# Kernel tuning notes

Hardware: AMD Instinct MI355X
Metric: run time of the kernel (lower is better)

Reference implementation:

```python
import jax, jax.numpy as jnp
import numpy as np

B, T, HID, H, Dk, Dv, K = 2, 1024, 1024, 8, 128, 128, 4
EPS = 1e-5


def _dwconv_causal(y, w, b):
    # y: [B,T,C], w: [C,1,K], b: [C]; torch Conv1d(padding=K-1) then [:, :, :T] == causal left-pad
    C = y.shape[-1]
    z = jnp.transpose(y, (0, 2, 1))  # [B,C,T]
    z = jax.lax.conv_general_dilated(
        z, w, window_strides=(1,), padding=[(K - 1, 0)],
        feature_group_count=C, dimension_numbers=("NCH", "OIH", "NCH"))
    z = z + b[None, :, None]
    return jnp.transpose(z, (0, 2, 1))


def _forward(x, Wq, Wk, Wv, conv_q_w, conv_q_b, conv_k_w, conv_k_b,
             conv_v_w, conv_v_b, Wa, ba, Wb, bb, Wg, Wo, ln_g, ln_b):
    b_, t_ = x.shape[0], x.shape[1]
    q = jax.nn.silu(_dwconv_causal(x @ Wq, conv_q_w, conv_q_b))
    k = jax.nn.silu(_dwconv_causal(x @ Wk, conv_k_w, conv_k_b))
    v = jax.nn.silu(_dwconv_causal(x @ Wv, conv_v_w, conv_v_b))
    q = q.reshape(b_, t_, H, Dk)
    k = k.reshape(b_, t_, H, Dk) * (Dk ** -0.5)
    v = v.reshape(b_, t_, H, Dv)
    alpha = jax.nn.sigmoid(x @ Wa + ba)  # [B,T,H]
    beta = jax.nn.sigmoid(x @ Wb + bb)   # [B,T,H]

    # time-major for scan
    qt = jnp.transpose(q, (1, 0, 2, 3))  # [T,B,H,Dk]
    kt = jnp.transpose(k, (1, 0, 2, 3))
    vt = jnp.transpose(v, (1, 0, 2, 3))  # [T,B,H,Dv]
    at = jnp.transpose(alpha, (1, 0, 2))  # [T,B,H]
    bt = jnp.transpose(beta, (1, 0, 2))

    def step(S, inp):
        q_t, k_t, v_t, a_t, b_t = inp
        sk = jnp.einsum('bhij,bhj->bhi', S, k_t)          # S @ k
        err = sk - v_t                                     # [B,H,Dv]
        S = a_t[:, :, None, None] * S - b_t[:, :, None, None] * (err[..., None] * k_t[:, :, None, :])
        o_t = jnp.einsum('bhij,bhj->bhi', S, q_t)          # S @ q (post-update)
        return S, o_t

    S0 = jnp.zeros((b_, H, Dv, Dk), x.dtype)
    _, o = jax.lax.scan(step, S0, (qt, kt, vt, at, bt))
    o = jnp.transpose(o, (1, 0, 2, 3))  # [B,T,H,Dv]

    # LayerNorm over Dv
    mu = jnp.mean(o, axis=-1, keepdims=True)
    var = jnp.mean((o - mu) ** 2, axis=-1, keepdims=True)
    o = (o - mu) * jax.lax.rsqrt(var + EPS) * ln_g + ln_b

    g = jax.nn.sigmoid(x @ Wg).reshape(b_, t_, H, Dv)
    o = (o * g).reshape(b_, t_, H * Dv)
    return o @ Wo


def setup_inputs() -> dict:
    key = jax.random.key(0)
    ks = jax.random.split(key, 18)
    s = 0.02

    def n(k, shape, scale=s):
        return jax.random.normal(k, shape, jnp.float32) * scale

    return {
        "x": jax.random.normal(ks[0], (B, T, HID), jnp.float32),
        "Wq": n(ks[1], (HID, H * Dk)),
        "Wk": n(ks[2], (HID, H * Dk)),
        "Wv": n(ks[3], (HID, H * Dv)),
        "conv_q_w": n(ks[4], (H * Dk, 1, K), 0.25),
        "conv_q_b": n(ks[5], (H * Dk,), 0.1),
        "conv_k_w": n(ks[6], (H * Dk, 1, K), 0.25),
        "conv_k_b": n(ks[7], (H * Dk,), 0.1),
        "conv_v_w": n(ks[8], (H * Dv, 1, K), 0.25),
        "conv_v_b": n(ks[9], (H * Dv,), 0.1),
        "Wa": n(ks[10], (HID, H)),
        "ba": n(ks[11], (H,), 0.1),
        "Wb": n(ks[12], (HID, H)),
        "bb": n(ks[13], (H,), 0.1),
        "Wg": n(ks[14], (HID, H * Dv)),
        "Wo": n(ks[15], (H * Dv, HID)),
        "ln_g": jnp.ones((Dv,), jnp.float32),
        "ln_b": jnp.zeros((Dv,), jnp.float32),
    }


def reference(x, Wq, Wk, Wv, conv_q_w, conv_q_b, conv_k_w, conv_k_b,
              conv_v_w, conv_v_b, Wa, ba, Wb, bb, Wg, Wo, ln_g, ln_b):
    return _forward(x, Wq, Wk, Wv, conv_q_w, conv_q_b, conv_k_w, conv_k_b,
                    conv_v_w, conv_v_b, Wa, ba, Wb, bb, Wg, Wo, ln_g, ln_b)
```

## Files before the change

### kernel.cpp

```cpp
#include <hip/hip_runtime.h>

#define TSEQ 1024
#define HID_ 1024
#define NH 8
#define DK 128
#define DV 128
#define ROWS 2048
#define SZf (ROWS * HID_)
#define LCH 64
#define NCK 16
#define KSTR 136
#define ESTR 65

typedef __attribute__((ext_vector_type(8))) short short8;
typedef __attribute__((ext_vector_type(4))) float f32x4;
#define MFMA __builtin_amdgcn_mfma_f32_16x16x32_bf16

__device__ __forceinline__ float sig_(float x) { return 1.f / (1.f + __expf(-x)); }

__device__ __forceinline__ ushort f2bf(float f) {
    unsigned int u = __builtin_bit_cast(unsigned int, f);
    u += 0x7FFF + ((u >> 16) & 1);
    return (ushort)(u >> 16);
}
__device__ __forceinline__ unsigned int pk2(float lo, float hi) {
    return (unsigned int)f2bf(lo) | ((unsigned int)f2bf(hi) << 16);
}

__global__ __launch_bounds__(256)
void k_wT(const float* __restrict__ s0, const float* __restrict__ s1,
          const float* __restrict__ s2, const float* __restrict__ s3,
          ushort* __restrict__ dst)
{
    const int z = blockIdx.z;
    const float* W = (z == 0) ? s0 : (z == 1) ? s1 : (z == 2) ? s2 : s3;
    ushort* WT = dst + (size_t)z * (1024 * 1024);
    __shared__ float t[64][65];
    const int n0 = blockIdx.x * 64, k0 = blockIdx.y * 64;
    const int rr = threadIdx.x >> 4, cc = threadIdx.x & 15;
#pragma unroll
    for (int i = 0; i < 4; ++i) {
        const int row = i * 16 + rr;
        float4 v = *(const float4*)(W + (size_t)(k0 + row) * 1024 + n0 + cc * 4);
        t[row][cc * 4 + 0] = v.x; t[row][cc * 4 + 1] = v.y;
        t[row][cc * 4 + 2] = v.z; t[row][cc * 4 + 3] = v.w;
    }
    __syncthreads();
#pragma unroll
    for (int i = 0; i < 4; ++i) {
        const int n = i * 16 + rr;
        const int kc = cc * 4;
        ushort4 o;
        o.x = f2bf(t[kc + 0][n]); o.y = f2bf(t[kc + 1][n]);
        o.z = f2bf(t[kc + 2][n]); o.w = f2bf(t[kc + 3][n]);
        *(ushort4*)(WT + (size_t)(n0 + n) * 1024 + k0 + kc) = o;
    }
}

#define LDSB 40
__device__ __forceinline__ void gemm_tile_mfma(const float* __restrict__ A,
                                               const ushort* __restrict__ BT,
                                               float* __restrict__ C,
                                               int brow, int bcol)
{
    __shared__ ushort As[128 * LDSB];
    __shared__ ushort Bs[128 * LDSB];
    const int tid  = threadIdx.x;
    const int lane = tid & 63;
    const int wv   = tid >> 6;
    const int wm   = (wv >> 1) * 64;
    const int wn   = (wv & 1) * 64;
    const int l15  = lane & 15;
    const int k8   = (lane >> 4) * 8;
    const int srow = tid >> 1;
    const int skh  = (tid & 1) * 16;

    f32x4 acc[4][4];
#pragma unroll
    for (int i = 0; i < 4; ++i)
#pragma unroll
        for (int j = 0; j < 4; ++j)
#pragma unroll
            for (int e = 0; e < 4; ++e) acc[i][j][e] = 0.f;

    const float*  arow = A  + (size_t)(brow + srow) * 1024 + skh;
    const ushort* brp  = BT + (size_t)(bcol + srow) * 1024 + skh;
    ushort* asw = As + srow * LDSB + skh;
    ushort* bsw = Bs + srow * LDSB + skh;

    for (int k0 = 0; k0 < 1024; k0 += 32) {
        float4 a0 = *(const float4*)(arow + k0);
        float4 a1 = *(const float4*)(arow + k0 + 4);
        float4 a2 = *(const float4*)(arow + k0 + 8);
        float4 a3 = *(const float4*)(arow + k0 + 12);
        uint4 b0 = *(const uint4*)(brp + k0);
        uint4 b1 = *(const uint4*)(brp + k0 + 8);
        uint4 w0, w1;
        w0.x = pk2(a0.x, a0.y); w0.y = pk2(a0.z, a0.w);
        w0.z = pk2(a1.x, a1.y); w0.w = pk2(a1.z, a1.w);
        w1.x = pk2(a2.x, a2.y); w1.y = pk2(a2.z, a2.w);
        w1.z = pk2(a3.x, a3.y); w1.w = pk2(a3.z, a3.w);
        __syncthreads();
        *(uint4*)(asw)     = w0;
        *(uint4*)(asw + 8) = w1;
        *(uint4*)(bsw)     = b0;
        *(uint4*)(bsw + 8) = b1;
        __syncthreads();
        short8 af[4], bf[4];
#pragma unroll
        for (int i = 0; i < 4; ++i)
            af[i] = *(const short8*)(As + (wm + i * 16 + l15) * LDSB + k8);
#pragma unroll
        for (int j = 0; j < 4; ++j)
            bf[j] = *(const short8*)(Bs + (wn + j * 16 + l15) * LDSB + k8);
#pragma unroll
        for (int i = 0; i < 4; ++i)
#pragma unroll
            for (int j = 0; j < 4; ++j)
                acc[i][j] = MFMA(af[i], bf[j], acc[i][j], 0, 0, 0);
    }
    const int l4 = lane >> 4;
#pragma unroll
    for (int i = 0; i < 4; ++i)
#pragma unroll
        for (int j = 0; j < 4; ++j)
#pragma unroll
            for (int r = 0; r < 4; ++r)
                C[(size_t)(brow + wm + i * 16 + l4 * 4 + r) * 1024 +
                  bcol + wn + j * 16 + l15] = acc[i][j][r];
}

__global__ __launch_bounds__(256)
void k_gemm4(const float* __restrict__ A, const ushort* __restrict__ WT,
             float* __restrict__ Cbase)
{
    const ushort* BT = WT + (size_t)blockIdx.z * (1024 * 1024);
    float* C = Cbase + (size_t)blockIdx.z * SZf;
    gemm_tile_mfma(A, BT, C, blockIdx.y * 128, blockIdx.x * 128);
}

__global__ __launch_bounds__(256)
void k_gemm1(const float* __restrict__ A, const ushort* __restrict__ BT,
             float* __restrict__ C)
{
    gemm_tile_mfma(A, BT, C, blockIdx.y * 128, blockIdx.x * 128);
}

__global__ __launch_bounds__(64)
void k_ab(const float* __restrict__ x, const float* __restrict__ Wa,
          const float* __restrict__ ba, const float* __restrict__ Wb,
          const float* __restrict__ bb, float* __restrict__ aT,
          float* __restrict__ bT)
{
    const int r = blockIdx.x;
    const int lane = threadIdx.x;
    const int b = r >> 10, t = r & 1023;
    const float* xr = x + (size_t)r * HID_;
    float acc[16];
#pragma unroll
    for (int n = 0; n < 16; ++n) acc[n] = 0.f;
    for (int c = lane; c < HID_; c += 64) {
        const float xv = xr[c];
        const float* wa = Wa + c * 8;
        const float* wb = Wb + c * 8;
#pragma unroll
        for (int n = 0; n < 8; ++n) {
            acc[n]     = fmaf(xv, wa[n], acc[n]);
            acc[8 + n] = fmaf(xv, wb[n], acc[8 + n]);
        }
    }
#pragma unroll
    for (int n = 0; n < 16; ++n) {
#pragma unroll
        for (int m = 32; m; m >>= 1) acc[n] += __shfl_xor(acc[n], m);
    }
    if (lane < 8) {
        aT[(size_t)(b * 8 + lane) * TSEQ + t] = sig_(acc[lane] + ba[lane]);
        bT[(size_t)(b * 8 + lane) * TSEQ + t] = sig_(acc[8 + lane] + bb[lane]);
    }
}

__global__ __launch_bounds__(256)
void k_conv_save(const float* __restrict__ q, const float* __restrict__ k,
                 const float* __restrict__ v, float* __restrict__ scr)
{
    const int z = blockIdx.z, b = blockIdx.y, j = blockIdx.x + 1;
    const float* y = (z == 0) ? q : (z == 1) ? k : v;
    float* d = scr + ((size_t)(z * 2 + b) * 15 + (j - 1)) * 3 * 1024;
    const float* s = y + ((size_t)b * TSEQ + j * 64 - 3) * HID_;
    for (int i = threadIdx.x; i < 3 * 1024; i += 256)
        d[i] = s[i];
}

__global__ __launch_bounds__(256)
void k_conv_apply(float* __restrict__ q, float* __restrict__ k, float* __restrict__ v,
                  const float* __restrict__ scr,
                  const float* __restrict__ wq, const float* __restrict__ bq,
                  const float* __restrict__ wk, const float* __restrict__ bk,
                  const float* __restrict__ wv, const float* __restrict__ bv)
{
    const int z = blockIdx.z, b = blockIdx.y;
    const int j = blockIdx.x >> 2, cg = blockIdx.x & 3;
    float* y          = (z == 0) ? q  : (z == 1) ? k  : v;
    const float* w    = (z == 0) ? wq : (z == 1) ? wk : wv;
    const float* bias = (z == 0) ? bq : (z == 1) ? bk : bv;
    const float scale = (z == 1) ? 0.08838834764831845f : 1.f;
    const int c = cg * 256 + threadIdx.x;
    const float w0 = w[c * 4], w1 = w[c * 4 + 1], w2 = w[c * 4 + 2], w3 = w[c * 4 + 3];
    const float bs = bias[c];
    float y0 = 0.f, y1 = 0.f, y2 = 0.f;
    if (j > 0) {
        const float* s = scr + ((size_t)(z * 2 + b) * 15 + (j - 1)) * 3 * 1024 + c;
        y0 = s[0]; y1 = s[1024]; y2 = s[2048];
    }
    float* yp = y + ((size_t)b * TSEQ + j * 64) * HID_ + c;
#pragma unroll 4
    for (int t = 0; t < 64; ++t) {
        float y3  = yp[(size_t)t * HID_];
        float acc = fmaf(w0, y0, fmaf(w1, y1, fmaf(w2, y2, fmaf(w3, y3, bs))));
        float sv  = acc * sig_(acc) * scale;
        yp[(size_t)t * HID_] = sv;
        y0 = y1; y1 = y2; y2 = y3;
    }
}

__global__ __launch_bounds__(256)
void k_prep(const float* __restrict__ klin, const float* __restrict__ qlin,
            const float* __restrict__ aT, const float* __restrict__ bT,
            ushort* __restrict__ Mg, ushort* __restrict__ Gg,
            float* __restrict__ pug, float* __restrict__ pog,
            float* __restrict__ cg, float* __restrict__ dtotg)
{
    const int cid = blockIdx.x;
    const int bh = cid >> 4, c = cid & 15;
    const int b = bh >> 3, h = bh & 7;
    const int tid = threadIdx.x;
    const int t0 = c * LCH;

    __shared__ ushort Kb[64 * KSTR], Qb[64 * KSTR];
    __shared__ float Ef[64 * ESTR];
    __shared__ float Mf[64 * ESTR];
    __shared__ float cums[64], bv[64];

    if (tid < 64) {
        const float a = aT[(size_t)bh * TSEQ + t0 + tid];
        bv[tid] = bT[(size_t)bh * TSEQ + t0 + tid];
        float cs = __logf(a);
#pragma unroll
        for (int d = 1; d < 64; d <<= 1) {
            float pv = __shfl_up(cs, d);
            if (tid >= d) cs += pv;
        }
        cums[tid] = cs;
    }
    const float* kb = klin + ((size_t)b * TSEQ + t0) * HID_ + h * DK;
    const float* qb = qlin + ((size_t)b * TSEQ + t0) * HID_ + h * DK;
#pragma unroll
    for (int j = 0; j < 8; ++j) {
        const int i4 = tid + j * 256;
        const int row = i4 >> 5, c4 = i4 & 31;
        float4 kv = *(const float4*)(kb + (size_t)row * HID_ + c4 * 4);
        float4 qv = *(const float4*)(qb + (size_t)row * HID_ + c4 * 4);
        uint2 kp; kp.x = pk2(kv.x, kv.y); kp.y = pk2(kv.z, kv.w);
        uint2 qp; qp.x = pk2(qv.x, qv.y); qp.y = pk2(qv.z, qv.w);
        *(uint2*)(Kb + row * KSTR + c4 * 4) = kp;
        *(uint2*)(Qb + row * KSTR + c4 * 4) = qp;
    }
    __syncthreads();

    const int wv = tid >> 6, l = tid & 63, l15 = l & 15, lq = l >> 4;
    const int k8o = lq * 8;
    f32x4 accK[4], accQ4[4];
#pragma unroll
    for (int j = 0; j < 4; ++j) {
        accK[j] = f32x4{0.f, 0.f, 0.f, 0.f};
        accQ4[j] = f32x4{0.f, 0.f, 0.f, 0.f};
    }
#pragma unroll
    for (int kk = 0; kk < 4; ++kk) {
        short8 aK = *(const short8*)(Kb + (wv * 16 + l15) * KSTR + kk * 32 + k8o);
        short8 aQ = *(const short8*)(Qb + (wv * 16 + l15) * KSTR + kk * 32 + k8o);
#pragma unroll
        for (int js = 0; js < 4; ++js) {
            short8 bK = *(const short8*)(Kb + (js * 16 + l15) * KSTR + kk * 32 + k8o);
            accK[js]  = MFMA(aK, bK, accK[js], 0, 0, 0);
            accQ4[js] = MFMA(aQ, bK, accQ4[js], 0, 0, 0);
        }
    }
    ushort* Gc = Gg + (size_t)cid * 4096;
#pragma unroll
    for (int js = 0; js < 4; ++js) {
#pragma unroll
        for (int r = 0; r < 4; ++r) {
            const int t = wv * 16 + lq * 4 + r;
            const int s = js * 16 + l15;
            const float cp = (t > 0) ? cums[t - 1] : 0.f;
            Ef[t * ESTR + s] = (s < t) ? __expf(cp - cums[s]) * accK[js][r] : 0.f;
            const float gv = (s <= t) ? __expf(cums[t] - cums[s]) * accQ4[js][r] : 0.f;
            Gc[t * 64 + s] = f2bf(gv);
        }
    }
    __syncthreads();

    if (tid < 64) {
        const int s = tid;
        for (int r = 0; r < 64; ++r) Mf[r * ESTR + s] = 0.f;
        Mf[s * ESTR + s] = bv[s];
        for (int t = 1; t < 64; ++t) {
            float s0 = 0.f, s1 = 0.f;
            int r = 0;
            for (; r + 1 < t; r += 2) {
                s0 = fmaf(Ef[t * ESTR + r],     Mf[r * ESTR + s],       s0);
                s1 = fmaf(Ef[t * ESTR + r + 1], Mf[(r + 1) * ESTR + s], s1);
            }
            if (r < t) s0 = fmaf(Ef[t * ESTR + r], Mf[r * ESTR + s], s0);
            if (s < t) Mf[t * ESTR + s] = -bv[t] * (s0 + s1);
        }
    }
    __syncthreads();
    ushort* Mc = Mg + (size_t)cid * 4096;
#pragma unroll
    for (int j = 0; j < 16; ++j) {
        const int e = tid + j * 256;
        Mc[e] = f2bf(Mf[(e >> 6) * ESTR + (e & 63)]);
    }
    if (tid < 64) {
        const float cp = (tid > 0) ? cums[tid - 1] : 0.f;
        pug[cid * 64 + tid] = __expf(cp);
        pog[cid * 64 + tid] = __expf(cums[tid]);
        cg [cid * 64 + tid] = __expf(cums[63] - cums[tid]);
        if (tid == 0) dtotg[cid] = __expf(cums[63]);
    }
}

__global__ __launch_bounds__(256)
void k_scan2(const float* __restrict__ klin, const float* __restrict__ qlin,
             const float* __restrict__ vlin,
             const ushort* __restrict__ Mg, const ushort* __restrict__ Gg,
             const float* __restrict__ pug, const float* __restrict__ pog,
             const float* __restrict__ cg, const float* __restrict__ dtotg,
             float* __restrict__ o)
{
    const int blk = blockIdx.x;
    const int bh = blk >> 2, rb = blk & 3;
    const int b = bh >> 3, h = bh & 7;
    const int tid = threadIdx.x;
    const int wv = tid >> 6, l = tid & 63, l15 = l & 15, lq = l >> 4;
    const int k8o = lq * 8;

    __shared__ ushort Kb[64 * KSTR], Qb[64 * KSTR];
    __shared__ ushort KTb[128 * 72];
    __shared__ float  Vtf[32 * 72];
    __shared__ ushort Mb[64 * 72], Gb[64 * 72];
    __shared__ ushort Shb[32 * KSTR], Slb[32 * KSTR];
    __shared__ ushort Yb[32 * 72], Wb[32 * 72], Wcb[32 * 72];
    __shared__ float  Otf[64 * 36];
    __shared__ float  puv[64], pov[64], cv2[64], dts[1];

    const int trow  = wv >> 1;
    const int tcol0 = (wv & 1) * 2;
    const int scol0 = (wv & 1) * 4;

    f32x4 accS[4];
#pragma unroll
    for (int m = 0; m < 4; ++m) accS[m] = f32x4{0.f, 0.f, 0.f, 0.f};

    const float* kbase = klin + (size_t)b * TSEQ * HID_ + h * DK;
    const float* qbase = qlin + (size_t)b * TSEQ * HID_ + h * DK;
    const float* vbase = vlin + (size_t)b * TSEQ * HID_ + h * DV + rb * 32;
    float* obase = o + (size_t)bh * TSEQ * DV + rb * 32;

    for (int c = 0; c < NCK; ++c) {
        const int cid = bh * 16 + c;
        const int t0 = c * LCH;
#pragma unroll
        for (int j = 0; j < 8; ++j) {
            const int i4 = tid + j * 256;
            const int row = i4 >> 5, c4 = i4 & 31;
            float4 kv = *(const float4*)(kbase + (size_t)(t0 + row) * HID_ + c4 * 4);
            float4 qv = *(const float4*)(qbase + (size_t)(t0 + row) * HID_ + c4 * 4);
            uint2 kp; kp.x = pk2(kv.x, kv.y); kp.y = pk2(kv.z, kv.w);
            uint2 qp; qp.x = pk2(qv.x, qv.y); qp.y = pk2(qv.z, qv.w);
            *(uint2*)(Kb + row * KSTR + c4 * 4) = kp;
            *(uint2*)(Qb + row * KSTR + c4 * 4) = qp;
            KTb[(c4 * 4 + 0) * 72 + row] = (ushort)(kp.x & 0xffffu);
            KTb[(c4 * 4 + 1) * 72 + row] = (ushort)(kp.x >> 16);
            KTb[(c4 * 4 + 2) * 72 + row] = (ushort)(kp.y & 0xffffu);
            KTb[(c4 * 4 + 3) * 72 + row] = (ushort)(kp.y >> 16);
        }
#pragma unroll
        for (int j = 0; j < 2; ++j) {
            const int i4 = tid + j * 256;
            const int row = i4 >> 3, c4 = i4 & 7;
            float4 vv = *(const float4*)(vbase + (size_t)(t0 + row) * HID_ + c4 * 4);
            Vtf[(c4 * 4 + 0) * 72 + row] = vv.x;
            Vtf[(c4 * 4 + 1) * 72 + row] = vv.y;
            Vtf[(c4 * 4 + 2) * 72 + row] = vv.z;
            Vtf[(c4 * 4 + 3) * 72 + row] = vv.w;
        }
        const ushort* Mc = Mg + (size_t)cid * 4096;
        const ushort* Gc = Gg + (size_t)cid * 4096;
#pragma unroll
        for (int j = 0; j < 2; ++j) {
            const int i8 = tid + j * 256;
            const int row = i8 >> 3, c8 = i8 & 7;
            *(uint4*)(Mb + row * 72 + c8 * 8) = *(const uint4*)(Mc + row * 64 + c8 * 8);
            *(uint4*)(Gb + row * 72 + c8 * 8) = *(const uint4*)(Gc + row * 64 + c8 * 8);
        }
        if (tid < 64) {
            puv[tid] = pug[cid * 64 + tid];
            pov[tid] = pog[cid * 64 + tid];
            cv2[tid] = cg[cid * 64 + tid];
            if (tid == 0) dts[0] = dtotg[cid];
        }
        __syncthreads();

#pragma unroll
        for (int m = 0; m < 4; ++m) {
#pragma unroll
            for (int r = 0; r < 4; ++r) {
                const int dv = trow * 16 + lq * 4 + r;
                const int dk = (scol0 + m) * 16 + l15;
                const float sv = accS[m][r];
                const ushort hi = f2bf(sv);
                const float hf = __builtin_bit_cast(float, ((unsigned)hi) << 16);
                Shb[dv * KSTR + dk] = hi;
                Slb[dv * KSTR + dk] = f2bf(sv - hf);
            }
        }
        __syncthreads();

        f32x4 accU[2], accQ[2];
#pragma unroll
        for (int jj = 0; jj < 2; ++jj) {
            accU[jj] = f32x4{0.f, 0.f, 0.f, 0.f};
            accQ[jj] = f32x4{0.f, 0.f, 0.f, 0.f};
        }
#pragma unroll
        for (int kk = 0; kk < 4; ++kk) {
            short8 ah = *(const short8*)(Shb + (trow * 16 + l15) * KSTR + kk * 32 + k8o);
            short8 al = *(const short8*)(Slb + (trow * 16 + l15) * KSTR + kk * 32 + k8o);
#pragma unroll
            for (int jj = 0; jj < 2; ++jj) {
                short8 bk = *(const short8*)(Kb + ((tcol0 + jj) * 16 + l15) * KSTR + kk * 32 + k8o);
                short8 bq = *(const short8*)(Qb + ((tcol0 + jj) * 16 + l15) * KSTR + kk * 32 + k8o);
                accU[jj] = MFMA(ah, bk, accU[jj], 0, 0, 0);
                accU[jj] = MFMA(al, bk, accU[jj], 0, 0, 0);
                accQ[jj] = MFMA(ah, bq, accQ[jj], 0, 0, 0);
                accQ[jj] = MFMA(al, bq, accQ[jj], 0, 0, 0);
            }
        }
#pragma unroll
        for (int jj = 0; jj < 2; ++jj) {
#pragma unroll
            for (int r = 0; r < 4; ++r) {
                const int t = (tcol0 + jj) * 16 + l15;
                const int dv = trow * 16 + lq * 4 + r;
                const float y = Vtf[dv * 72 + t] - puv[t] * accU[jj][r];
                Yb[dv * 72 + t] = f2bf(y);
            }
        }
        __syncthreads();

        f32x4 accW[2];
#pragma unroll
        for (int jj = 0; jj < 2; ++jj) accW[jj] = f32x4{0.f, 0.f, 0.f, 0.f};
#pragma unroll
        for (int kk = 0; kk < 2; ++kk) {
            short8 ay = *(const short8*)(Yb + (trow * 16 + l15) * 72 + kk * 32 + k8o);
#pragma unroll
            for (int jj = 0; jj < 2; ++jj) {
                short8 bm = *(const short8*)(Mb + ((tcol0 + jj) * 16 + l15) * 72 + kk * 32 + k8o);
                accW[jj] = MFMA(ay, bm, accW[jj], 0, 0, 0);
            }
        }
#pragma unroll
        for (int jj = 0; jj < 2; ++jj) {
#pragma unroll
            for (int r = 0; r < 4; ++r) {
                const int t = (tcol0 + jj) * 16 + l15;
                const int dv = trow * 16 + lq * 4 + r;
                const float wvl = accW[jj][r];
                Wb[dv * 72 + t]  = f2bf(wvl);
                Wcb[dv * 72 + t] = f2bf(wvl * cv2[t]);
            }
        }
        __syncthreads();

        f32x4 accO[2];
#pragma unroll
        for (int jj = 0; jj < 2; ++jj) accO[jj] = f32x4{0.f, 0.f, 0.f, 0.f};
#pragma unroll
        for (int kk = 0; kk < 2; ++kk) {
            short8 aw = *(const short8*)(Wb + (trow * 16 + l15) * 72 + kk * 32 + k8o);
#pragma unroll
            for (int jj = 0; jj < 2; ++jj) {
                short8 bg = *(const short8*)(Gb + ((tcol0 + jj) * 16 + l15) * 72 + kk * 32 + k8o);
                accO[jj] = MFMA(aw, bg, accO[jj], 0, 0, 0);
            }
        }
#pragma unroll
        for (int jj = 0; jj < 2; ++jj) {
#pragma unroll
            for (int r = 0; r < 4; ++r) {
                const int t = (tcol0 + jj) * 16 + l15;
                const int dv = trow * 16 + lq * 4 + r;
                Otf[t * 36 + dv] = pov[t] * accQ[jj][r] + accO[jj][r];
            }
        }
        const float dt = dts[0];
#pragma unroll
        for (int m = 0; m < 4; ++m)
#pragma unroll
            for (int r = 0; r < 4; ++r) accS[m][r] *= dt;
#pragma unroll
        for (int kk = 0; kk < 2; ++kk) {
            short8 aw = *(const short8*)(Wcb + (trow * 16 + l15) * 72 + kk * 32 + k8o);
#pragma unroll
            for (int m = 0; m < 4; ++m) {
                short8 bk = *(const short8*)(KTb + ((scol0 + m) * 16 + l15) * 72 + kk * 32 + k8o);
                accS[m] = MFMA(aw, bk, accS[m], 0, 0, 0);
            }
        }
        __syncthreads();

#pragma unroll
        for (int j = 0; j < 2; ++j) {
            const int i4 = tid + j * 256;
            const int row = i4 >> 3, c4 = i4 & 7;
            float4 ov = *(const float4*)(Otf + row * 36 + c4 * 4);
            *(float4*)(obase + (size_t)(t0 + row) * DV + c4 * 4) = ov;
        }
        __syncthreads();
    }
}

__global__ __launch_bounds__(256)
void k_ln_gate(const float* __restrict__ o, const float* __restrict__ g_lin,
               const float* __restrict__ ln_g, const float* __restrict__ ln_b,
               float* __restrict__ og)
{
    const int idx  = blockIdx.x * 4 + (threadIdx.x >> 6);
    const int lane = threadIdx.x & 63;
    const int h  = idx & 7;
    const int bt = idx >> 3;
    const int b  = bt >> 10;
    const int t  = bt & 1023;
    const float* op = o + ((size_t)(b * NH + h) * TSEQ + t) * DV;
    float2 xv = ((const float2*)op)[lane];
    float s = xv.x + xv.y;
#pragma unroll
    for (int m = 32; m; m >>= 1) s += __shfl_xor(s, m);
    const float mu = s * (1.f / 128.f);
    const float d0 = xv.x - mu, d1 = xv.y - mu;
    float v = d0 * d0 + d1 * d1;
#pragma unroll
    for (int m = 32; m; m >>= 1) v += __shfl_xor(v, m);
    const float inv = rsqrtf(v * (1.f / 128.f) + 1e-5f);
    const int d = lane * 2;
    const float* gp = g_lin + (size_t)bt * HID_ + h * DV;
    const float g0 = sig_(gp[d]), g1 = sig_(gp[d + 1]);
    const float y0 = (d0 * inv * ln_g[d]     + ln_b[d])     * g0;
    const float y1 = (d1 * inv * ln_g[d + 1] + ln_b[d + 1]) * g1;
    ((float2*)(og + (size_t)bt * HID_ + h * DV))[lane] = make_float2(y0, y1);
}

extern "C" void kernel_launch(void* const* d_in, const int* in_sizes, int n_in,
                              void* d_out, int out_size, void* d_ws, size_t ws_size,
                              hipStream_t stream)
{
    const float* x   = (const float*)d_in[0];
    const float* Wq  = (const float*)d_in[1];
    const float* Wk  = (const float*)d_in[2];
    const float* Wv  = (const float*)d_in[3];
    const float* cqw = (const float*)d_in[4];
    const float* cqb = (const float*)d_in[5];
    const float* ckw = (const float*)d_in[6];
    const float* ckb = (const float*)d_in[7];
    const float* cvw = (const float*)d_in[8];
    const float* cvb = (const float*)d_in[9];
    const float* Wa  = (const float*)d_in[10];
    const float* ba  = (const float*)d_in[11];
    const float* Wb  = (const float*)d_in[12];
    const float* bb  = (const float*)d_in[13];
    const float* Wg  = (const float*)d_in[14];
    const float* Wo  = (const float*)d_in[15];
    const float* lng = (const float*)d_in[16];
    const float* lnb = (const float*)d_in[17];
    float* out = (float*)d_out;
    float* ws  = (float*)d_ws;

    float* q_lin = ws;
    float* k_lin = ws + 1 * (size_t)SZf;
    float* v_lin = ws + 2 * (size_t)SZf;
    float* g_lin = ws + 3 * (size_t)SZf;
    float* o_buf = ws + 4 * (size_t)SZf;
    float* aT    = ws + 5 * (size_t)SZf;
    float* bT    = aT + 16 * TSEQ;
    float* pug   = bT + 16 * TSEQ;
    float* pog   = pug + 256 * 64;
    float* cgd   = pog + 256 * 64;
    float* dtg   = cgd + 256 * 64;
    float* og    = ws;

    ushort* WT4 = (ushort*)o_buf;
    ushort* WoT = (ushort*)k_lin;
    ushort* Mg  = (ushort*)out;
    ushort* Gg  = Mg + 256 * 4096;

    k_wT<<<dim3(16, 16, 4), 256, 0, stream>>>(Wq, Wk, Wv, Wg, WT4);
    k_gemm4<<<dim3(8, 16, 4), 256, 0, stream>>>(x, WT4, ws);
    k_ab<<<ROWS, 64, 0, stream>>>(x, Wa, ba, Wb, bb, aT, bT);
    k_conv_save<<<dim3(15, 2, 3), 256, 0, stream>>>(q_lin, k_lin, v_lin, o_buf);
    k_conv_apply<<<dim3(64, 2, 3), 256, 0, stream>>>(q_lin, k_lin, v_lin, o_buf,
                                                     cqw, cqb, ckw, ckb, cvw, cvb);
    k_prep<<<256, 256, 0, stream>>>(k_lin, q_lin, aT, bT, Mg, Gg, pug, pog, cgd, dtg);
    k_scan2<<<64, 256, 0, stream>>>(k_lin, q_lin, v_lin, Mg, Gg, pug, pog, cgd, dtg, o_buf);
    k_wT<<<dim3(16, 16, 1), 256, 0, stream>>>(Wo, Wo, Wo, Wo, WoT);
    k_ln_gate<<<4096, 256, 0, stream>>>(o_buf, g_lin, lng, lnb, og);
    k_gemm1<<<dim3(8, 16), 256, 0, stream>>>(og, WoT, out);
}
```

Before: 249.3 us.

## Pre-stage bf16 operands and double-buffer chunk loads in the scan kernel

Converts x to bf16 once so the GEMMs load bf16 A tiles directly. A new staging kernel packs K, Q and transposed K per chunk into bf16 buffers that are reused by the prep and scan kernels. The scan kernel now prefetches the next chunk into registers while computing the current one. The LN/gate output is written as bf16 for the final GEMM. This cuts fp32 traffic and conversion work and hides scan load latency, at the cost of an extra kernel, more workspace and higher register pressure in the scan.

```diff
diff --git a/kernel.cpp b/kernel.cpp
--- a/kernel.cpp
+++ b/kernel.cpp
@@ -28,6 +28,18 @@
 }
 
 __global__ __launch_bounds__(256)
+void k_x2bf(const float* __restrict__ x, ushort* __restrict__ xb)
+{
+    const size_t i8 = (size_t)blockIdx.x * 256 + threadIdx.x;
+    float4 v0 = *(const float4*)(x + i8 * 8);
+    float4 v1 = *(const float4*)(x + i8 * 8 + 4);
+    uint4 o;
+    o.x = pk2(v0.x, v0.y); o.y = pk2(v0.z, v0.w);
+    o.z = pk2(v1.x, v1.y); o.w = pk2(v1.z, v1.w);
+    *(uint4*)(xb + i8 * 8) = o;
+}
+
+__global__ __launch_bounds__(256)
 void k_wT(const float* __restrict__ s0, const float* __restrict__ s1,
           const float* __restrict__ s2, const float* __restrict__ s3,
           ushort* __restrict__ dst)
@@ -58,7 +70,7 @@
 }
 
 #define LDSB 40
-__device__ __forceinline__ void gemm_tile_mfma(const float* __restrict__ A,
+__device__ __forceinline__ void gemm_tile_mfma(const ushort* __restrict__ A,
                                                const ushort* __restrict__ BT,
                                                float* __restrict__ C,
                                                int brow, int bcol)
@@ -83,26 +95,19 @@
 #pragma unroll
             for (int e = 0; e < 4; ++e) acc[i][j][e] = 0.f;
 
-    const float*  arow = A  + (size_t)(brow + srow) * 1024 + skh;
+    const ushort* arow = A  + (size_t)(brow + srow) * 1024 + skh;
     const ushort* brp  = BT + (size_t)(bcol + srow) * 1024 + skh;
     ushort* asw = As + srow * LDSB + skh;
     ushort* bsw = Bs + srow * LDSB + skh;
 
     for (int k0 = 0; k0 < 1024; k0 += 32) {
-        float4 a0 = *(const float4*)(arow + k0);
-        float4 a1 = *(const float4*)(arow + k0 + 4);
-        float4 a2 = *(const float4*)(arow + k0 + 8);
-        float4 a3 = *(const float4*)(arow + k0 + 12);
+        uint4 a0 = *(const uint4*)(arow + k0);
+        uint4 a1 = *(const uint4*)(arow + k0 + 8);
         uint4 b0 = *(const uint4*)(brp + k0);
         uint4 b1 = *(const uint4*)(brp + k0 + 8);
-        uint4 w0, w1;
-        w0.x = pk2(a0.x, a0.y); w0.y = pk2(a0.z, a0.w);
-        w0.z = pk2(a1.x, a1.y); w0.w = pk2(a1.z, a1.w);
-        w1.x = pk2(a2.x, a2.y); w1.y = pk2(a2.z, a2.w);
-        w1.z = pk2(a3.x, a3.y); w1.w = pk2(a3.z, a3.w);
         __syncthreads();
-        *(uint4*)(asw)     = w0;
-        *(uint4*)(asw + 8) = w1;
+        *(uint4*)(asw)     = a0;
+        *(uint4*)(asw + 8) = a1;
         *(uint4*)(bsw)     = b0;
         *(uint4*)(bsw + 8) = b1;
         __syncthreads();
@@ -131,7 +136,7 @@
 }
 
 __global__ __launch_bounds__(256)
-void k_gemm4(const float* __restrict__ A, const ushort* __restrict__ WT,
+void k_gemm4(const ushort* __restrict__ A, const ushort* __restrict__ WT,
              float* __restrict__ Cbase)
 {
     const ushort* BT = WT + (size_t)blockIdx.z * (1024 * 1024);
@@ -140,7 +145,7 @@
 }
 
 __global__ __launch_bounds__(256)
-void k_gemm1(const float* __restrict__ A, const ushort* __restrict__ BT,
+void k_gemm1(const ushort* __restrict__ A, const ushort* __restrict__ BT,
              float* __restrict__ C)
 {
     gemm_tile_mfma(A, BT, C, blockIdx.y * 128, blockIdx.x * 128);
@@ -225,36 +230,19 @@
 }
 
 __global__ __launch_bounds__(256)
-void k_prep(const float* __restrict__ klin, const float* __restrict__ qlin,
-            const float* __restrict__ aT, const float* __restrict__ bT,
-            ushort* __restrict__ Mg, ushort* __restrict__ Gg,
-            float* __restrict__ pug, float* __restrict__ pog,
-            float* __restrict__ cg, float* __restrict__ dtotg)
+void k_stage(const float* __restrict__ klin, const float* __restrict__ qlin,
+             ushort* __restrict__ Kst, ushort* __restrict__ Qst,
+             ushort* __restrict__ KTst)
 {
     const int cid = blockIdx.x;
     const int bh = cid >> 4, c = cid & 15;
     const int b = bh >> 3, h = bh & 7;
     const int tid = threadIdx.x;
     const int t0 = c * LCH;
-
-    __shared__ ushort Kb[64 * KSTR], Qb[64 * KSTR];
-    __shared__ float Ef[64 * ESTR];
-    __shared__ float Mf[64 * ESTR];
-    __shared__ float cums[64], bv[64];
-
-    if (tid < 64) {
-        const float a = aT[(size_t)bh * TSEQ + t0 + tid];
-        bv[tid] = bT[(size_t)bh * TSEQ + t0 + tid];
-        float cs = __logf(a);
-#pragma unroll
-        for (int d = 1; d < 64; d <<= 1) {
-            float pv = __shfl_up(cs, d);
-            if (tid >= d) cs += pv;
-        }
-        cums[tid] = cs;
-    }
+    __shared__ ushort Kl[64 * KSTR];
     const float* kb = klin + ((size_t)b * TSEQ + t0) * HID_ + h * DK;
     const float* qb = qlin + ((size_t)b * TSEQ + t0) * HID_ + h * DK;
+    const size_t go = (size_t)cid * 8192;
 #pragma unroll
     for (int j = 0; j < 8; ++j) {
         const int i4 = tid + j * 256;
@@ -263,8 +251,57 @@
         float4 qv = *(const float4*)(qb + (size_t)row * HID_ + c4 * 4);
         uint2 kp; kp.x = pk2(kv.x, kv.y); kp.y = pk2(kv.z, kv.w);
         uint2 qp; qp.x = pk2(qv.x, qv.y); qp.y = pk2(qv.z, qv.w);
-        *(uint2*)(Kb + row * KSTR + c4 * 4) = kp;
-        *(uint2*)(Qb + row * KSTR + c4 * 4) = qp;
+        *(uint2*)(Kst + go + row * 128 + c4 * 4) = kp;
+        *(uint2*)(Qst + go + row * 128 + c4 * 4) = qp;
+        *(uint2*)(Kl + row * KSTR + c4 * 4) = kp;
+    }
+    __syncthreads();
+#pragma unroll
+    for (int j = 0; j < 4; ++j) {
+        const int o8 = tid + j * 256;
+        const int dk = o8 >> 3, tt = (o8 & 7) * 8;
+        ushort tmp[8];
+#pragma unroll
+        for (int e = 0; e < 8; ++e) tmp[e] = Kl[(tt + e) * KSTR + dk];
+        *(uint4*)(KTst + go + dk * 64 + tt) = *(uint4*)tmp;
+    }
+}
+
+__global__ __launch_bounds__(256)
+void k_prep(const ushort* __restrict__ Kst, const ushort* __restrict__ Qst,
+            const float* __restrict__ aT, const float* __restrict__ bT,
+            ushort* __restrict__ Mg, ushort* __restrict__ Gg,
+            float* __restrict__ pug, float* __restrict__ pog,
+            float* __restrict__ cg, float* __restrict__ dtotg)
+{
+    const int cid = blockIdx.x;
+    const int bh = cid >> 4, c = cid & 15;
+    const int tid = threadIdx.x;
+    const int t0 = c * LCH;
+
+    __shared__ ushort Kb[64 * KSTR], Qb[64 * KSTR];
+    __shared__ float Ef[64 * ESTR];
+    __shared__ float Mf[64 * ESTR];
+    __shared__ float cums[64], bv[64];
+
+    if (tid < 64) {
+        const float a = aT[(size_t)bh * TSEQ + t0 + tid];
+        bv[tid] = bT[(size_t)bh * TSEQ + t0 + tid];
+        float cs = __logf(a);
+#pragma unroll
+        for (int d = 1; d < 64; d <<= 1) {
+            float pv = __shfl_up(cs, d);
+            if (tid >= d) cs += pv;
+        }
+        cums[tid] = cs;
+    }
+    const size_t go = (size_t)cid * 8192;
+#pragma unroll
+    for (int j = 0; j < 4; ++j) {
+        const int i16 = tid + j * 256;
+        const int row = i16 >> 4, col = (i16 & 15) * 8;
+        *(uint4*)(Kb + row * KSTR + col) = *(const uint4*)(Kst + go + i16 * 8);
+        *(uint4*)(Qb + row * KSTR + col) = *(const uint4*)(Qst + go + i16 * 8);
     }
     __syncthreads();
 
@@ -334,8 +371,8 @@
 }
 
 __global__ __launch_bounds__(256)
-void k_scan2(const float* __restrict__ klin, const float* __restrict__ qlin,
-             const float* __restrict__ vlin,
+void k_scan2(const ushort* __restrict__ Kst, const ushort* __restrict__ Qst,
+             const ushort* __restrict__ KTst, const float* __restrict__ vlin,
              const ushort* __restrict__ Mg, const ushort* __restrict__ Gg,
              const float* __restrict__ pug, const float* __restrict__ pog,
              const float* __restrict__ cg, const float* __restrict__ dtotg,
@@ -365,55 +402,69 @@
 #pragma unroll
     for (int m = 0; m < 4; ++m) accS[m] = f32x4{0.f, 0.f, 0.f, 0.f};
 
-    const float* kbase = klin + (size_t)b * TSEQ * HID_ + h * DK;
-    const float* qbase = qlin + (size_t)b * TSEQ * HID_ + h * DK;
     const float* vbase = vlin + (size_t)b * TSEQ * HID_ + h * DV + rb * 32;
     float* obase = o + (size_t)bh * TSEQ * DV + rb * 32;
 
-    for (int c = 0; c < NCK; ++c) {
-        const int cid = bh * 16 + c;
-        const int t0 = c * LCH;
-#pragma unroll
-        for (int j = 0; j < 8; ++j) {
+    uint4 rk[4], rq[4], rkt[4], rm[2], rg[2];
+    float4 rv[2];
+    float rpu = 0.f, rpo = 0.f, rcv = 0.f, rdt = 0.f;
+
+    auto LOADC = [&](int cc) {
+        const int cid = bh * 16 + cc;
+        const size_t go = (size_t)cid * 8192;
+#pragma unroll
+        for (int j = 0; j < 4; ++j) {
+            rk[j]  = *(const uint4*)(Kst  + go + (tid + j * 256) * 8);
+            rq[j]  = *(const uint4*)(Qst  + go + (tid + j * 256) * 8);
+            rkt[j] = *(const uint4*)(KTst + go + (tid + j * 256) * 8);
+        }
+#pragma unroll
+        for (int j = 0; j < 2; ++j) {
+            rm[j] = *(const uint4*)(Mg + (size_t)cid * 4096 + (tid + j * 256) * 8);
+            rg[j] = *(const uint4*)(Gg + (size_t)cid * 4096 + (tid + j * 256) * 8);
             const int i4 = tid + j * 256;
-            const int row = i4 >> 5, c4 = i4 & 31;
-            float4 kv = *(const float4*)(kbase + (size_t)(t0 + row) * HID_ + c4 * 4);
-            float4 qv = *(const float4*)(qbase + (size_t)(t0 + row) * HID_ + c4 * 4);
-            uint2 kp; kp.x = pk2(kv.x, kv.y); kp.y = pk2(kv.z, kv.w);
-            uint2 qp; qp.x = pk2(qv.x, qv.y); qp.y = pk2(qv.z, qv.w);
-            *(uint2*)(Kb + row * KSTR + c4 * 4) = kp;
-            *(uint2*)(Qb + row * KSTR + c4 * 4) = qp;
-            KTb[(c4 * 4 + 0) * 72 + row] = (ushort)(kp.x & 0xffffu);
-            KTb[(c4 * 4 + 1) * 72 + row] = (ushort)(kp.x >> 16);
-            KTb[(c4 * 4 + 2) * 72 + row] = (ushort)(kp.y & 0xffffu);
-            KTb[(c4 * 4 + 3) * 72 + row] = (ushort)(kp.y >> 16);
+            rv[j] = *(const float4*)(vbase + (size_t)(cc * LCH + (i4 >> 3)) * HID_ + (i4 & 7) * 4);
+        }
+        if (tid < 64) {
+            rpu = pug[cid * 64 + tid];
+            rpo = pog[cid * 64 + tid];
+            rcv = cg [cid * 64 + tid];
+            if (tid == 0) rdt = dtotg[cid];
+        }
+    };
+    auto WRITEC = [&]() {
+#pragma unroll
+        for (int j = 0; j < 4; ++j) {
+            const int i16 = tid + j * 256;
+            *(uint4*)(Kb  + (i16 >> 4) * KSTR + (i16 & 15) * 8) = rk[j];
+            *(uint4*)(Qb  + (i16 >> 4) * KSTR + (i16 & 15) * 8) = rq[j];
+            *(uint4*)(KTb + (i16 >> 3) * 72   + (i16 & 7) * 8)  = rkt[j];
         }
 #pragma unroll
         for (int j = 0; j < 2; ++j) {
+            const int i8 = tid + j * 256;
+            *(uint4*)(Mb + (i8 >> 3) * 72 + (i8 & 7) * 8) = rm[j];
+            *(uint4*)(Gb + (i8 >> 3) * 72 + (i8 & 7) * 8) = rg[j];
             const int i4 = tid + j * 256;
             const int row = i4 >> 3, c4 = i4 & 7;
-            float4 vv = *(const float4*)(vbase + (size_t)(t0 + row) * HID_ + c4 * 4);
-            Vtf[(c4 * 4 + 0) * 72 + row] = vv.x;
-            Vtf[(c4 * 4 + 1) * 72 + row] = vv.y;
-            Vtf[(c4 * 4 + 2) * 72 + row] = vv.z;
-            Vtf[(c4 * 4 + 3) * 72 + row] = vv.w;
-        }
-        const ushort* Mc = Mg + (size_t)cid * 4096;
-        const ushort* Gc = Gg + (size_t)cid * 4096;
-#pragma unroll
-        for (int j = 0; j < 2; ++j) {
-            const int i8 = tid + j * 256;
-            const int row = i8 >> 3, c8 = i8 & 7;
-            *(uint4*)(Mb + row * 72 + c8 * 8) = *(const uint4*)(Mc + row * 64 + c8 * 8);
-            *(uint4*)(Gb + row * 72 + c8 * 8) = *(const uint4*)(Gc + row * 64 + c8 * 8);
+            Vtf[(c4 * 4 + 0) * 72 + row] = rv[j].x;
+            Vtf[(c4 * 4 + 1) * 72 + row] = rv[j].y;
+            Vtf[(c4 * 4 + 2) * 72 + row] = rv[j].z;
+            Vtf[(c4 * 4 + 3) * 72 + row] = rv[j].w;
         }
         if (tid < 64) {
-            puv[tid] = pug[cid * 64 + tid];
-            pov[tid] = pog[cid * 64 + tid];
-            cv2[tid] = cg[cid * 64 + tid];
-            if (tid == 0) dts[0] = dtotg[cid];
-        }
-        __syncthreads();
+            puv[tid] = rpu; pov[tid] = rpo; cv2[tid] = rcv;
+            if (tid == 0) dts[0] = rdt;
+        }
+    };
+
+    LOADC(0);
+    WRITEC();
+    __syncthreads();
+
+    for (int c = 0; c < NCK; ++c) {
+        const int t0 = c * LCH;
+        if (c + 1 < NCK) LOADC(c + 1);
 
 #pragma unroll
         for (int m = 0; m < 4; ++m) {
@@ -531,6 +582,7 @@
             float4 ov = *(const float4*)(Otf + row * 36 + c4 * 4);
             *(float4*)(obase + (size_t)(t0 + row) * DV + c4 * 4) = ov;
         }
+        if (c + 1 < NCK) WRITEC();
         __syncthreads();
     }
 }
@@ -538,7 +590,7 @@
 __global__ __launch_bounds__(256)
 void k_ln_gate(const float* __restrict__ o, const float* __restrict__ g_lin,
                const float* __restrict__ ln_g, const float* __restrict__ ln_b,
-               float* __restrict__ og)
+               ushort* __restrict__ ogb)
 {
     const int idx  = blockIdx.x * 4 + (threadIdx.x >> 6);
     const int lane = threadIdx.x & 63;
@@ -562,7 +614,7 @@
     const float g0 = sig_(gp[d]), g1 = sig_(gp[d + 1]);
     const float y0 = (d0 * inv * ln_g[d]     + ln_b[d])     * g0;
     const float y1 = (d1 * inv * ln_g[d + 1] + ln_b[d + 1]) * g1;
-    ((float2*)(og + (size_t)bt * HID_ + h * DV))[lane] = make_float2(y0, y1);
+    *(uint*)(ogb + (size_t)bt * HID_ + h * DV + d) = pk2(y0, y1);
 }
 
 extern "C" void kernel_launch(void* const* d_in, const int* in_sizes, int n_in,
@@ -601,22 +653,31 @@
     float* pog   = pug + 256 * 64;
     float* cgd   = pog + 256 * 64;
     float* dtg   = cgd + 256 * 64;
-    float* og    = ws;
+
+    float*  tail = ws + 5 * (size_t)SZf + 131072;
+    ushort* Kst  = (ushort*)tail;
+    ushort* Qst  = Kst + (size_t)256 * 8192;
+    ushort* xbf  = Qst + (size_t)256 * 8192;
 
     ushort* WT4 = (ushort*)o_buf;
     ushort* WoT = (ushort*)k_lin;
+    ushort* ogb = (ushort*)q_lin;
     ushort* Mg  = (ushort*)out;
-    ushort* Gg  = Mg + 256 * 4096;
-
+    ushort* Gg  = Mg + (size_t)256 * 4096;
+    ushort* KTst = Gg + (size_t)256 * 4096;
+
+    k_x2bf<<<1024, 256, 0, stream>>>(x, xbf);
     k_wT<<<dim3(16, 16, 4), 256, 0, stream>>>(Wq, Wk, Wv, Wg, WT4);
-    k_gemm4<<<dim3(8, 16, 4), 256, 0, stream>>>(x, WT4, ws);
+    k_gemm4<<<dim3(8, 16, 4), 256, 0, stream>>>(xbf, WT4, ws);
     k_ab<<<ROWS, 64, 0, stream>>>(x, Wa, ba, Wb, bb, aT, bT);
     k_conv_save<<<dim3(15, 2, 3), 256, 0, stream>>>(q_lin, k_lin, v_lin, o_buf);
     k_conv_apply<<<dim3(64, 2, 3), 256, 0, stream>>>(q_lin, k_lin, v_lin, o_buf,
                                                      cqw, cqb, ckw, ckb, cvw, cvb);
-    k_prep<<<256, 256, 0, stream>>>(k_lin, q_lin, aT, bT, Mg, Gg, pug, pog, cgd, dtg);
-    k_scan2<<<64, 256, 0, stream>>>(k_lin, q_lin, v_lin, Mg, Gg, pug, pog, cgd, dtg, o_buf);
+    k_stage<<<256, 256, 0, stream>>>(k_lin, q_lin, Kst, Qst, KTst);
+    k_prep<<<256, 256, 0, stream>>>(Kst, Qst, aT, bT, Mg, Gg, pug, pog, cgd, dtg);
     k_wT<<<dim3(16, 16, 1), 256, 0, stream>>>(Wo, Wo, Wo, Wo, WoT);
-    k_ln_gate<<<4096, 256, 0, stream>>>(o_buf, g_lin, lng, lnb, og);
-    k_gemm1<<<dim3(8, 16), 256, 0, stream>>>(og, WoT, out);
-}
+    k_scan2<<<64, 256, 0, stream>>>(Kst, Qst, KTst, v_lin, Mg, Gg,
+                                    pug, pog, cgd, dtg, o_buf);
+    k_ln_gate<<<4096, 256, 0, stream>>>(o_buf, g_lin, lng, lnb, ogb);
+    k_gemm1<<<dim3(8, 16), 256, 0, stream>>>(ogb, WoT, out);
+}
```

Result: faster. 230.4 us (-7.6%).
